# Performance work log

Hardware: AMD Instinct MI355X
Metric: run time of the kernel (lower is better)

## Reference

```python
import jax, jax.numpy as jnp
import numpy as np

N_NODES, N_EDGES, BATCH = 50000, 100000, 256
H = 64            # dim_hidden_features
D_NODE, D_EDGE, D_RBF = 110, 8, 8
D_SET = 2 * H     # Set2Set input_dim = 128, output_dim = 256
D_HID = 512
D_CAT = 54
MP_STEPS, S2S_ITERS = 4, 3


def setup_inputs() -> dict:
    key = jax.random.key(0)
    ks = iter(jax.random.split(key, 48))

    def nrm(shape, s=0.05):
        return jax.random.normal(next(ks), shape, dtype=jnp.float32) * s

    inp = {}
    inp["node_attribute"] = jax.random.normal(next(ks), (N_NODES, D_NODE), dtype=jnp.float32)
    inp["edge_attribute"] = jax.random.normal(next(ks), (N_EDGES, D_EDGE), dtype=jnp.float32)
    inp["edge_length"] = jax.random.uniform(next(ks), (N_EDGES,), dtype=jnp.float32)
    inp["src"] = jax.random.randint(next(ks), (N_EDGES,), 0, N_NODES, dtype=jnp.int32)
    inp["dst"] = jax.random.randint(next(ks), (N_EDGES,), 0, N_NODES, dtype=jnp.int32)
    inp["node_graph"] = jnp.sort(jax.random.randint(next(ks), (N_NODES,), 0, BATCH, dtype=jnp.int32))
    # atom_feature_projector
    inp["proj_W"] = nrm((D_NODE, H)); inp["proj_b"] = jnp.zeros((H,), jnp.float32)
    # RBF layer: centers ~ U(0,1), beta = 10 (per reset_parameters)
    inp["centers"] = jax.random.uniform(next(ks), (D_RBF,), dtype=jnp.float32)
    inp["beta"] = jnp.full((D_RBF,), 10.0, jnp.float32)
    # NNConv edge function: Linear(16 -> 64*64), plus NNConv bias
    inp["bond_W"] = nrm((D_EDGE + D_RBF, H * H)); inp["bond_b"] = jnp.zeros((H * H,), jnp.float32)
    inp["conv_b"] = jnp.zeros((H,), jnp.float32)
    # GRU (input H, hidden H); PyTorch layout (3H, in)
    inp["gru_Wih"] = nrm((3 * H, H)); inp["gru_Whh"] = nrm((3 * H, H))
    inp["gru_bih"] = jnp.zeros((3 * H,), jnp.float32); inp["gru_bhh"] = jnp.zeros((3 * H,), jnp.float32)
    # Set2Set LSTM: input 2*D_SET=256, hidden D_SET=128, 2 layers; PyTorch layout (4H, in)
    inp["lstm_Wih0"] = nrm((4 * D_SET, 2 * D_SET)); inp["lstm_Whh0"] = nrm((4 * D_SET, D_SET))
    inp["lstm_bih0"] = jnp.zeros((4 * D_SET,), jnp.float32); inp["lstm_bhh0"] = jnp.zeros((4 * D_SET,), jnp.float32)
    inp["lstm_Wih1"] = nrm((4 * D_SET, D_SET)); inp["lstm_Whh1"] = nrm((4 * D_SET, D_SET))
    inp["lstm_bih1"] = jnp.zeros((4 * D_SET,), jnp.float32); inp["lstm_bhh1"] = jnp.zeros((4 * D_SET,), jnp.float32)
    # sparsify: Linear(256 -> 512) + PReLU(init 0.25)
    inp["sp_W"] = nrm((2 * D_SET, D_HID)); inp["sp_b"] = jnp.zeros((D_HID,), jnp.float32)
    inp["prelu_a"] = jnp.array([0.25], jnp.float32)
    # catalyst1 head: hiddens[0] (512->512 ReLU, 512->512 Tanh) then outputs[0] (512->54)
    inp["h0_W1"] = nrm((D_HID, D_HID)); inp["h0_b1"] = jnp.zeros((D_HID,), jnp.float32)
    inp["h0_W2"] = nrm((D_HID, D_HID)); inp["h0_b2"] = jnp.zeros((D_HID,), jnp.float32)
    inp["out_W"] = nrm((D_HID, D_CAT)); inp["out_b"] = jnp.zeros((D_CAT,), jnp.float32)
    return inp


def _lstm_cell(x, h, c, Wih, Whh, bih, bhh):
    # PyTorch LSTM gate order: i, f, g, o
    g = x @ Wih.T + bih + h @ Whh.T + bhh
    i, f, gg, o = jnp.split(g, 4, axis=-1)
    c = jax.nn.sigmoid(f) * c + jax.nn.sigmoid(i) * jnp.tanh(gg)
    h = jax.nn.sigmoid(o) * jnp.tanh(c)
    return h, c


def reference(node_attribute, edge_attribute, edge_length, src, dst, node_graph,
              proj_W, proj_b, centers, beta, bond_W, bond_b, conv_b,
              gru_Wih, gru_Whh, gru_bih, gru_bhh,
              lstm_Wih0, lstm_Whh0, lstm_bih0, lstm_bhh0,
              lstm_Wih1, lstm_Whh1, lstm_bih1, lstm_bhh1,
              sp_W, sp_b, prelu_a, h0_W1, h0_b1, h0_W2, h0_b2, out_W, out_b):
    n_nodes = node_attribute.shape[0]
    # atom feature projection
    x = jax.nn.relu(node_attribute @ proj_W + proj_b)                       # (N, H)
    # edge features = [edge_attribute, RBF(length)]
    rbf = jnp.exp(-beta * (edge_length[:, None] - centers[None, :]) ** 2)   # (E, 8)
    efeat = jnp.concatenate([edge_attribute, rbf], axis=-1)                 # (E, 16)
    # NNConv per-edge weight matrix; edge features are constant over MP steps
    W_e = (efeat @ bond_W + bond_b).reshape(-1, H, H)                       # (E, H, H)

    feat, h = x, x
    for _ in range(MP_STEPS):
        # NNConv: message = h_src @ W_e, sum-aggregated at dst, plus bias
        m = jnp.einsum('ei,eio->eo', feat[src], W_e)                        # (E, H)
        agg = jax.ops.segment_sum(m, dst, num_segments=n_nodes) + conv_b    # (N, H)
        gx = jax.nn.relu(agg)
        # GRU cell (PyTorch gate order r, z, n)
        gi = gx @ gru_Wih.T + gru_bih
        gh = h @ gru_Whh.T + gru_bhh
        i_r, i_z, i_n = jnp.split(gi, 3, axis=-1)
        h_r, h_z, h_n = jnp.split(gh, 3, axis=-1)
        r = jax.nn.sigmoid(i_r + h_r)
        z = jax.nn.sigmoid(i_z + h_z)
        n = jnp.tanh(i_n + r * h_n)
        h = (1.0 - z) * n + z * h
        feat = h
    node_agg = jnp.concatenate([feat, x], axis=-1)                          # (N, 2H)

    # Set2Set pooling over graphs (segment softmax attention, 2-layer LSTM)
    B = BATCH
    h0 = c0 = jnp.zeros((B, D_SET), node_agg.dtype)
    h1 = c1 = jnp.zeros((B, D_SET), node_agg.dtype)
    q_star = jnp.zeros((B, 2 * D_SET), node_agg.dtype)
    for _ in range(S2S_ITERS):
        h0, c0 = _lstm_cell(q_star, h0, c0, lstm_Wih0, lstm_Whh0, lstm_bih0, lstm_bhh0)
        h1, c1 = _lstm_cell(h0, h1, c1, lstm_Wih1, lstm_Whh1, lstm_bih1, lstm_bhh1)
        q = h1                                                              # (B, 128)
        e = jnp.sum(node_agg * q[node_graph], axis=-1)                      # (N,)
        emax = jax.ops.segment_max(e, node_graph, num_segments=B)
        p = jnp.exp(e - emax[node_graph])
        denom = jax.ops.segment_sum(p, node_graph, num_segments=B)
        alpha = p / denom[node_graph]                                       # per-graph softmax
        r_out = jax.ops.segment_sum(node_agg * alpha[:, None], node_graph, num_segments=B)
        q_star = jnp.concatenate([q, r_out], axis=-1)                       # (B, 256)

    # sparsify (Linear + PReLU)
    feats = q_star @ sp_W + sp_b                                            # (B, 512)
    feats = jnp.where(feats >= 0, feats, prelu_a * feats)
    # catalyst1 head
    hid = jnp.tanh(jax.nn.relu(feats @ h0_W1 + h0_b1) @ h0_W2 + h0_b2)
    return jax.nn.softmax(hid @ out_W + out_b, axis=-1)                     # (B, 54)
```

## Files before the change

kernel.cpp:

```cpp
#include <hip/hip_runtime.h>
#include <math.h>

constexpr int N = 50000;
constexpr int E = 100000;
constexpr int B = 256;
constexpr int H = 64;
constexpr int DN = 110;
constexpr int NBLK = (E + 63) / 64;

#define DEV __device__ __forceinline__

typedef __attribute__((ext_vector_type(8))) short short8;
typedef __attribute__((ext_vector_type(4))) float floatx4;

DEV float sigf(float x) { return 1.0f / (1.0f + expf(-x)); }

DEV short f2bf(float f) {
    unsigned u = __float_as_uint(f);
    unsigned r = (u + 0x7fffu + ((u >> 16) & 1u)) >> 16;
    return (short)r;
}
DEV float bf2f(short s) { return __uint_as_float(((unsigned)(unsigned short)s) << 16); }

DEV void cvt8(const float* p, short8& hi, short8& lo) {
    float4 u0 = *(const float4*)p;
    float4 u1 = *(const float4*)(p + 4);
    float vv[8] = {u0.x, u0.y, u0.z, u0.w, u1.x, u1.y, u1.z, u1.w};
#pragma unroll
    for (int j = 0; j < 8; ++j) {
        short hb = f2bf(vv[j]);
        hi[j] = hb;
        lo[j] = f2bf(vv[j] - bf2f(hb));
    }
}

__global__ void k_izero(int* p, int n) {
    int i = blockIdx.x * 256 + threadIdx.x;
    if (i < n) p[i] = 0;
}

DEV void d_packpair(const float* __restrict__ in, float* __restrict__ out, int IN_I, int idx) {
    int i = idx >> 8;
    int j = idx & 255;
    out[2 * idx]     = in[(size_t)j * IN_I + i];
    out[2 * idx + 1] = in[(size_t)(j + 256) * IN_I + i];
}

DEV void d_prepB(const float* __restrict__ W, short* __restrict__ out,
                 int NT16, int ld, int trans, int ocap, int kcap, int idx) {
    int lane = idx & 63;
    int t = idx >> 6;
    int ntile = t % NT16;
    int kt = t / NT16;
    int quad = lane >> 4, col = lane & 15;
    int o = ntile * 16 + col;
    short hi[8], lo[8];
#pragma unroll
    for (int j = 0; j < 8; ++j) {
        int k = kt * 32 + quad * 8 + j;
        float v = 0.0f;
        if (o < ocap && k < kcap) v = trans ? W[(size_t)o * ld + k] : W[(size_t)k * ld + o];
        short hb = f2bf(v);
        hi[j] = hb;
        lo[j] = f2bf(v - bf2f(hb));
    }
    short* dh = out + (((size_t)(t * 2 + 0) * 64 + lane) * 8);
    short* dl = out + (((size_t)(t * 2 + 1) * 64 + lane) * 8);
#pragma unroll
    for (int j = 0; j < 8; ++j) { dh[j] = hi[j]; dl[j] = lo[j]; }
}

DEV void d_prepW(const float* __restrict__ bond_W, const float* __restrict__ bond_b,
                 short* __restrict__ wf, int idx) {
    int lane = idx & 63;
    int t = idx >> 6;
    int ks = t & 1;
    int nt = (t >> 1) & 3;
    int kk = t >> 3;
    const float* S = (kk < 16) ? (bond_W + kk * 4096) : bond_b;
    int quad = lane >> 4, col = lane & 15;
    short hi[8], lo[8];
#pragma unroll
    for (int j = 0; j < 8; ++j) {
        int i = ks * 32 + quad * 8 + j;
        float v = S[i * 64 + nt * 16 + col];
        short hb = f2bf(v);
        hi[j] = hb;
        lo[j] = f2bf(v - bf2f(hb));
    }
    short* dh = wf + (((size_t)(t * 2 + 0) * 64 + lane) * 8);
    short* dl = wf + (((size_t)(t * 2 + 1) * 64 + lane) * 8);
#pragma unroll
    for (int j = 0; j < 8; ++j) { dh[j] = hi[j]; dl[j] = lo[j]; }
}

__launch_bounds__(256)
__global__ void k_prep0(const float* lWih0, const float* lWhh0, const float* lWih1, const float* lWhh1,
                        float* lW0P, float* lU0P, float* lW1P, float* lU1P,
                        const float* bond_W, const float* bond_b, short* wf,
                        const float* gru_Wih, const float* gru_Whh, short* fgI, short* fgH,
                        const float* proj_W, short* fproj,
                        const float* ea, const float* el, const float* centers,
                        const float* beta, const int* epos, float* ef_t,
                        const int* ng, int* gs, int* ge,
                        float* zreg) {
    int idx = blockIdx.x * 256 + threadIdx.x;
    if (idx < 65536) { d_packpair(lWih0, lW0P, 256, idx); return; }
    idx -= 65536;
    if (idx < 32768) { d_packpair(lWhh0, lU0P, 128, idx); return; }
    idx -= 32768;
    if (idx < 32768) { d_packpair(lWih1, lW1P, 128, idx); return; }
    idx -= 32768;
    if (idx < 32768) { d_packpair(lWhh1, lU1P, 128, idx); return; }
    idx -= 32768;
    if (idx < 8704) { d_prepW(bond_W, bond_b, wf, idx); return; }
    idx -= 8704;
    if (idx < 1536) { d_prepB(gru_Wih, fgI, 12, 64, 1, 192, 64, idx); return; }
    idx -= 1536;
    if (idx < 1536) { d_prepB(gru_Whh, fgH, 12, 64, 1, 192, 64, idx); return; }
    idx -= 1536;
    if (idx < 1024) { d_prepB(proj_W, fproj, 4, 64, 0, 64, DN, idx); return; }
    idx -= 1024;
    if (idx < E) {
        int e = idx;
        int pos = epos[e];
        float L = el[e];
#pragma unroll
        for (int j = 0; j < 8; ++j) ef_t[(size_t)j * E + pos] = ea[e * 8 + j];
#pragma unroll
        for (int j = 0; j < 8; ++j) {
            float d = L - centers[j];
            ef_t[(size_t)(8 + j) * E + pos] = expf(-beta[j] * d * d);
        }
        ef_t[(size_t)16 * E + pos] = 1.0f;
        return;
    }
    idx -= E;
    if (idx < N) {
        int n = idx;
        int g = ng[n];
        int gp = (n == 0) ? -1 : ng[n - 1];
        if (g != gp) {
            gs[g] = n;
            if (n > 0) ge[gp] = n;
            for (int q = gp + 1; q < g; ++q) { gs[q] = 0; ge[q] = 0; }
        }
        if (n == N - 1) {
            ge[g] = N;
            for (int q = g + 1; q < B; ++q) { gs[q] = 0; ge[q] = 0; }
        }
        return;
    }
    idx -= N;
    if (idx < 196608) { zreg[idx] = 0.0f; return; }
}
constexpr int PREP0_TOTAL = 65536 + 3 * 32768 + 8704 + 2 * 1536 + 1024 + E + N + 196608;

__launch_bounds__(256)
__global__ void k_prephead(const float* sp_W, short* fsp, const float* h0_W1, short* fw1,
                           const float* h0_W2, short* fw2, const float* out_W, short* fow) {
    int idx = blockIdx.x * 256 + threadIdx.x;
    if (idx < 16384) { d_prepB(sp_W, fsp, 32, 512, 0, 512, 256, idx); return; }
    idx -= 16384;
    if (idx < 32768) { d_prepB(h0_W1, fw1, 32, 512, 0, 512, 512, idx); return; }
    idx -= 32768;
    if (idx < 32768) { d_prepB(h0_W2, fw2, 32, 512, 0, 512, 512, idx); return; }
    idx -= 32768;
    if (idx < 4096) { d_prepB(out_W, fow, 4, 54, 0, 54, 512, idx); return; }
}
constexpr int PREPH_TOTAL = 16384 + 2 * 32768 + 4096;

__global__ void k_deg(const int* __restrict__ dst, int* __restrict__ deg) {
    int e = blockIdx.x * 256 + threadIdx.x;
    if (e < E) atomicAdd(&deg[dst[e]], 1);
}
__global__ void k_scan1(const int* __restrict__ deg, int* __restrict__ bsum) {
    __shared__ int s[256];
    int b = blockIdx.x, tid = threadIdx.x;
    int idx = b * 256 + tid;
    s[tid] = (idx < N) ? deg[idx] : 0;
    __syncthreads();
    for (int st = 128; st > 0; st >>= 1) {
        if (tid < st) s[tid] += s[tid + st];
        __syncthreads();
    }
    if (tid == 0) bsum[b] = s[0];
}
__global__ void k_scan2p(int* __restrict__ bsum, int nb) {
    __shared__ int s[256];
    int tid = threadIdx.x;
    int v = (tid < nb) ? bsum[tid] : 0;
    s[tid] = v;
    __syncthreads();
    for (int off = 1; off < 256; off <<= 1) {
        int t = (tid >= off) ? s[tid - off] : 0;
        __syncthreads();
        s[tid] += t;
        __syncthreads();
    }
    if (tid < nb) bsum[tid] = s[tid] - v;
}
__global__ void k_scan3(const int* __restrict__ deg, const int* __restrict__ bsum,
                        int* __restrict__ cursor, int* __restrict__ roff) {
    __shared__ int s[256];
    int b = blockIdx.x, tid = threadIdx.x;
    int idx = b * 256 + tid;
    int v = (idx < N) ? deg[idx] : 0;
    s[tid] = v;
    __syncthreads();
    for (int off = 1; off < 256; off <<= 1) {
        int t = (tid >= off) ? s[tid - off] : 0;
        __syncthreads();
        s[tid] += t;
        __syncthreads();
    }
    if (idx < N) {
        int start = bsum[b] + s[tid] - v;
        cursor[idx] = start;
        roff[idx] = start;
    }
    if (idx == 0) roff[N] = E;
}
__global__ void k_scat(const int* __restrict__ src, const int* __restrict__ dst,
                       int* __restrict__ cursor, int* __restrict__ srcp,
                       int* __restrict__ epos, int* __restrict__ dstp) {
    int e = blockIdx.x * 256 + threadIdx.x;
    if (e >= E) return;
    int d = dst[e];
    int pos = atomicAdd(&cursor[d], 1);
    srcp[pos] = src[e];
    dstp[pos] = d;
    epos[e] = pos;
}

__launch_bounds__(256)
__global__ void k_projm(const float* __restrict__ na, const short* __restrict__ fp,
                        const float* __restrict__ b, float* __restrict__ x,
                        short* __restrict__ hs) {
    __shared__ float as[16 * 132];
    int tid = threadIdx.x, lane = tid & 63, nt = tid >> 6;
    int quad = lane >> 4, col = lane & 15;
    int s0 = blockIdx.x * 16;
    for (int i = tid; i < 16 * DN; i += 256) {
        int r = i / DN, c = i % DN;
        as[r * 132 + c] = na[(size_t)s0 * DN + i];
    }
    for (int i = tid; i < 16 * 22; i += 256) {
        int r = i / 22, c = DN + i % 22;
        as[r * 132 + c] = 0.0f;
    }
    __syncthreads();
    const short8* F = (const short8*)fp;
    floatx4 T = {0.0f, 0.0f, 0.0f, 0.0f};
#pragma unroll
    for (int kt = 0; kt < 4; ++kt) {
        const float* ap = as + col * 132 + kt * 32 + quad * 8;
        short8 ah, al;
#pragma unroll
        for (int j = 0; j < 8; ++j) {
            float v = ap[j];
            short hb = f2bf(v);
            ah[j] = hb;
            al[j] = f2bf(v - bf2f(hb));
        }
        int t = kt * 4 + nt;
        short8 bh = F[(t * 2 + 0) * 64 + lane];
        short8 bl = F[(t * 2 + 1) * 64 + lane];
        T = __builtin_amdgcn_mfma_f32_16x16x32_bf16(ah, bh, T, 0, 0, 0);
        T = __builtin_amdgcn_mfma_f32_16x16x32_bf16(al, bh, T, 0, 0, 0);
        T = __builtin_amdgcn_mfma_f32_16x16x32_bf16(ah, bl, T, 0, 0, 0);
    }
    int o = nt * 16 + col;
    float bo = b[o];
#pragma unroll
    for (int r = 0; r < 4; ++r) {
        int n = s0 + quad * 4 + r;
        float v = fmaxf(T[r] + bo, 0.0f);
        x[(size_t)n * 64 + o] = v;
        short hb = f2bf(v);
        hs[(size_t)n * 128 + o] = hb;
        hs[(size_t)n * 128 + 64 + o] = f2bf(v - bf2f(hb));
    }
}

__launch_bounds__(256)
__global__ void k_msgagg(const short* __restrict__ hs, const float* __restrict__ ef_t,
                         const short* __restrict__ wf, const int* __restrict__ srcp,
                         const int* __restrict__ dstp,
                         float* __restrict__ agg, float* __restrict__ bpart) {
    __shared__ int dsh[64];
    __shared__ int shprev;
    __shared__ float Csh[64][68];

    int tid = threadIdx.x;
    int e0 = blockIdx.x * 64;
    int lane = tid & 63;
    int nt = tid >> 6;
    int quad = lane >> 4, col = lane & 15;

    if (tid < 64) {
        int eg = e0 + tid;
        dsh[tid] = (eg < E) ? dstp[eg] : N;
    }
    if (tid == 0) shprev = (e0 == 0) ? -1 : dstp[e0 - 1];

    short8 Ah[4][2], Al[4][2];
#pragma unroll
    for (int mt = 0; mt < 4; ++mt) {
        int eg = e0 + mt * 16 + col;
        int s = (eg < E) ? srcp[eg] : 0;
        const short* hp = hs + (size_t)s * 128 + quad * 8;
#pragma unroll
        for (int ks = 0; ks < 2; ++ks) {
            Ah[mt][ks] = *(const short8*)(hp + ks * 32);
            Al[mt][ks] = *(const short8*)(hp + 64 + ks * 32);
        }
    }

    const short8* Wf = (const short8*)wf;
    const float* efb = ef_t + e0 + quad * 4;
    float C[4][4] = {};

#define LOADB(d0, d1, d2, d3, KK)                      \
    {                                                  \
        int tb_ = ((KK) * 4 + nt) * 2;                 \
        d0 = Wf[((tb_ + 0) * 2 + 0) * 64 + lane];      \
        d1 = Wf[((tb_ + 1) * 2 + 0) * 64 + lane];      \
        d2 = Wf[((tb_ + 0) * 2 + 1) * 64 + lane];      \
        d3 = Wf[((tb_ + 1) * 2 + 1) * 64 + lane];      \
    }

    short8 c0, c1, c2, c3, n0_, n1_, n2_, n3_, q0, q1, q2, q3;
    LOADB(c0, c1, c2, c3, 0);
    LOADB(n0_, n1_, n2_, n3_, 1);
    LOADB(q0, q1, q2, q3, 2);

#pragma unroll 1
    for (int kk = 0; kk < 17; ++kk) {
        int kn = kk + 3;
        if (kn > 16) kn = 16;
        short8 p0, p1, p2, p3;
        LOADB(p0, p1, p2, p3, kn);

        float4 ef0 = *(const float4*)(efb + (size_t)kk * E + 0);
        float4 ef1 = *(const float4*)(efb + (size_t)kk * E + 16);
        float4 ef2 = *(const float4*)(efb + (size_t)kk * E + 32);
        float4 ef3 = *(const float4*)(efb + (size_t)kk * E + 48);
        float4 efv[4] = {ef0, ef1, ef2, ef3};

#pragma unroll
        for (int mt = 0; mt < 4; ++mt) {
            floatx4 T = {0.0f, 0.0f, 0.0f, 0.0f};
            T = __builtin_amdgcn_mfma_f32_16x16x32_bf16(Ah[mt][0], c0, T, 0, 0, 0);
            T = __builtin_amdgcn_mfma_f32_16x16x32_bf16(Ah[mt][1], c1, T, 0, 0, 0);
            T = __builtin_amdgcn_mfma_f32_16x16x32_bf16(Al[mt][0], c0, T, 0, 0, 0);
            T = __builtin_amdgcn_mfma_f32_16x16x32_bf16(Al[mt][1], c1, T, 0, 0, 0);
            T = __builtin_amdgcn_mfma_f32_16x16x32_bf16(Ah[mt][0], c2, T, 0, 0, 0);
            T = __builtin_amdgcn_mfma_f32_16x16x32_bf16(Ah[mt][1], c3, T, 0, 0, 0);
            C[mt][0] += efv[mt].x * T[0];
            C[mt][1] += efv[mt].y * T[1];
            C[mt][2] += efv[mt].z * T[2];
            C[mt][3] += efv[mt].w * T[3];
        }
        c0 = n0_; c1 = n1_; c2 = n2_; c3 = n3_;
        n0_ = q0; n1_ = q1; n2_ = q2; n3_ = q3;
        q0 = p0; q1 = p1; q2 = p2; q3 = p3;
    }
#undef LOADB

#pragma unroll
    for (int mt = 0; mt < 4; ++mt)
#pragma unroll
        for (int r = 0; r < 4; ++r)
            Csh[mt * 16 + quad * 4 + r][nt * 16 + col] = C[mt][r];
    __syncthreads();

    if (tid < 64) {
        int c = tid;
        int prevd = shprev;
        int firstd = dsh[0];
        for (int q = prevd + 1; q < firstd; ++q) agg[(size_t)q * 64 + c] = 0.0f;
        int cur = firstd;
        float acc = 0.0f;
        bool owned = (e0 == 0) || (firstd != prevd);
        bool done = false;
        for (int r = 0; r < 64; ++r) {
            int d = dsh[r];
            if (d != cur) {
                if (owned) agg[(size_t)cur * 64 + c] = acc;
                else bpart[(size_t)blockIdx.x * 64 + c] = acc;
                int dc = (d < N) ? d : N;
                for (int q = cur + 1; q < dc; ++q) agg[(size_t)q * 64 + c] = 0.0f;
                cur = d;
                acc = 0.0f;
                owned = true;
                if (cur >= N) { done = true; break; }
            }
            acc += Csh[r][c];
        }
        if (!done) {
            if (owned) agg[(size_t)cur * 64 + c] = acc;
            else bpart[(size_t)blockIdx.x * 64 + c] = acc;
        }
    }
}

__launch_bounds__(256)
__global__ void k_gru4(const float* agg, const float* __restrict__ bpart,
                       const int* __restrict__ roff, const float* __restrict__ conv_b,
                       short* __restrict__ hs,
                       const short* __restrict__ fI, const short* __restrict__ fH,
                       const float* __restrict__ bih, const float* __restrict__ bhh,
                       float* hf) {
    __shared__ float aggS[32 * 65];
    __shared__ short hsS[32 * 132];
    int tid = threadIdx.x, lane = tid & 63, nt = tid >> 6;
    int quad = lane >> 4, col = lane & 15;
    int n0 = blockIdx.x * 32;

    {
        const float* src = agg + (size_t)n0 * 64;
#pragma unroll
        for (int it = 0; it < 2; ++it) {
            int i = tid * 4 + it * 1024;
            float4 v = {0.0f, 0.0f, 0.0f, 0.0f};
            if ((size_t)n0 * 64 + i + 3 < (size_t)N * 64) v = *(const float4*)(src + i);
            int r = i >> 6, c = i & 63;
            *(float4*)&aggS[r * 65 + c] = v;
        }
        const short* hsrc = hs + (size_t)n0 * 128;
#pragma unroll
        for (int it = 0; it < 2; ++it) {
            int i = tid * 8 + it * 2048;
            short8 v = short8{0, 0, 0, 0, 0, 0, 0, 0};
            if ((size_t)n0 * 128 + i + 7 < (size_t)N * 128) v = *(const short8*)(hsrc + i);
            int r = i >> 7, c = i & 127;
            *(short8*)&hsS[r * 132 + c] = v;
        }
    }
    __syncthreads();

    short8 Gh[2][2], Gl[2][2], Hh[2][2], Hl[2][2];
#pragma unroll
    for (int mt = 0; mt < 2; ++mt) {
        int node = n0 + mt * 16 + col;
        bool ok = node < N;
        int row = mt * 16 + col;
        float acc[2][8];
        const float* ag = &aggS[row * 65];
#pragma unroll
        for (int ks = 0; ks < 2; ++ks) {
            const float* cb = conv_b + ks * 32 + quad * 8;
            float4 a0 = *(const float4*)(ag + ks * 32 + quad * 8);
            float4 a1 = *(const float4*)(ag + ks * 32 + quad * 8 + 4);
            acc[ks][0] = a0.x + cb[0]; acc[ks][1] = a0.y + cb[1];
            acc[ks][2] = a0.z + cb[2]; acc[ks][3] = a0.w + cb[3];
            acc[ks][4] = a1.x + cb[4]; acc[ks][5] = a1.y + cb[5];
            acc[ks][6] = a1.z + cb[6]; acc[ks][7] = a1.w + cb[7];
        }
        int rs = ok ? roff[node] : 0;
        int re = ok ? roff[node + 1] : 0;
        if (re > rs) {
            int b0 = rs >> 6, b1 = (re - 1) >> 6;
            for (int bb = b0 + 1; bb <= b1; ++bb) {
                const float* bp = bpart + (size_t)bb * 64;
#pragma unroll
                for (int ks = 0; ks < 2; ++ks) {
                    float4 p0 = *(const float4*)(bp + ks * 32 + quad * 8);
                    float4 p1 = *(const float4*)(bp + ks * 32 + quad * 8 + 4);
                    acc[ks][0] += p0.x; acc[ks][1] += p0.y;
                    acc[ks][2] += p0.z; acc[ks][3] += p0.w;
                    acc[ks][4] += p1.x; acc[ks][5] += p1.y;
                    acc[ks][6] += p1.z; acc[ks][7] += p1.w;
                }
            }
        }
        const short* hp = &hsS[row * 132];
#pragma unroll
        for (int ks = 0; ks < 2; ++ks) {
            Hh[mt][ks] = *(const short8*)(hp + ks * 32);
            Hl[mt][ks] = *(const short8*)(hp + 64 + ks * 32);
#pragma unroll
            for (int j = 0; j < 8; ++j) {
                float g = ok ? fmaxf(acc[ks][j], 0.0f) : 0.0f;
                short gb = f2bf(g);
                Gh[mt][ks][j] = gb;
                Gl[mt][ks][j] = f2bf(g - bf2f(gb));
            }
        }
    }
    __syncthreads();

    const short8* FI = (const short8*)fI;
    const short8* FH = (const short8*)fH;
    floatx4 aI[2][3] = {}, aH[2][3] = {};
#pragma unroll
    for (int ks = 0; ks < 2; ++ks) {
        short8 bIh[3], bIl[3], bHh[3], bHl[3];
#pragma unroll
        for (int g = 0; g < 3; ++g) {
            int t = ks * 12 + g * 4 + nt;
            bIh[g] = FI[(t * 2 + 0) * 64 + lane];
            bIl[g] = FI[(t * 2 + 1) * 64 + lane];
            bHh[g] = FH[(t * 2 + 0) * 64 + lane];
            bHl[g] = FH[(t * 2 + 1) * 64 + lane];
        }
#pragma unroll
        for (int mt = 0; mt < 2; ++mt) {
#pragma unroll
            for (int g = 0; g < 3; ++g) {
                aI[mt][g] = __builtin_amdgcn_mfma_f32_16x16x32_bf16(Gh[mt][ks], bIh[g], aI[mt][g], 0, 0, 0);
                aI[mt][g] = __builtin_amdgcn_mfma_f32_16x16x32_bf16(Gl[mt][ks], bIh[g], aI[mt][g], 0, 0, 0);
                aI[mt][g] = __builtin_amdgcn_mfma_f32_16x16x32_bf16(Gh[mt][ks], bIl[g], aI[mt][g], 0, 0, 0);
                aH[mt][g] = __builtin_amdgcn_mfma_f32_16x16x32_bf16(Hh[mt][ks], bHh[g], aH[mt][g], 0, 0, 0);
                aH[mt][g] = __builtin_amdgcn_mfma_f32_16x16x32_bf16(Hl[mt][ks], bHh[g], aH[mt][g], 0, 0, 0);
                aH[mt][g] = __builtin_amdgcn_mfma_f32_16x16x32_bf16(Hh[mt][ks], bHl[g], aH[mt][g], 0, 0, 0);
            }
        }
    }

    int o = nt * 16 + col;
    float br = bih[o], bz = bih[64 + o], bn = bih[128 + o];
    float cr = bhh[o], cz = bhh[64 + o], cn = bhh[128 + o];
#pragma unroll
    for (int mt = 0; mt < 2; ++mt) {
#pragma unroll
        for (int r = 0; r < 4; ++r) {
            int row = mt * 16 + quad * 4 + r;
            float rg = sigf(aI[mt][0][r] + br + aH[mt][0][r] + cr);
            float z  = sigf(aI[mt][1][r] + bz + aH[mt][1][r] + cz);
            float ng = tanhf(aI[mt][2][r] + bn + rg * (aH[mt][2][r] + cn));
            float hold = bf2f(hsS[row * 132 + o]) + bf2f(hsS[row * 132 + 64 + o]);
            aggS[row * 65 + o] = (1.0f - z) * ng + z * hold;
        }
    }
    __syncthreads();

#pragma unroll
    for (int it = 0; it < 2; ++it) {
        int i = tid * 8 + it * 2048;
        int r = i >> 7, c = i & 127;
        int node = n0 + r;
        if (node < N) {
            bool hiP = (c < 64);
            int f0 = hiP ? c : (c - 64);
            short8 v;
#pragma unroll
            for (int j = 0; j < 8; ++j) {
                float hv = aggS[r * 65 + f0 + j];
                short hb = f2bf(hv);
                v[j] = hiP ? hb : f2bf(hv - bf2f(hb));
            }
            *(short8*)(hs + (size_t)node * 128 + c) = v;
        }
    }
    if (hf) {
#pragma unroll
        for (int it = 0; it < 2; ++it) {
            int i = tid * 4 + it * 1024;
            int r = i >> 6, c = i & 63;
            int node = n0 + r;
            if (node < N)
                *(float4*)(hf + (size_t)node * 64 + c) = *(const float4*)&aggS[r * 65 + c];
        }
    }
}

__launch_bounds__(256)
__global__ void k_s2s(float* __restrict__ h0, float* __restrict__ c0,
                      float* __restrict__ h1, float* __restrict__ c1,
                      float* __restrict__ q_star,
                      const float* __restrict__ W0P, const float* __restrict__ U0P,
                      const float* __restrict__ b0i, const float* __restrict__ b0h,
                      const float* __restrict__ W1P, const float* __restrict__ U1P,
                      const float* __restrict__ b1i, const float* __restrict__ b1h,
                      const float* __restrict__ hf, const float* __restrict__ x,
                      const int* __restrict__ gs, const int* __restrict__ ge) {
    __shared__ float xb[256], hb[128], gb[512], h0n[128], qv[128];
    __shared__ float mrg[4][2][64];
    __shared__ float ml[4][2];
    int g = blockIdx.x, tid = threadIdx.x;
    xb[tid] = q_star[g * 256 + tid];
    if (tid < 128) hb[tid] = h0[g * 128 + tid];
    __syncthreads();
    float g0 = b0i[tid] + b0h[tid];
    float g1 = b0i[tid + 256] + b0h[tid + 256];
    for (int i = 0; i < 256; ++i) {
        float xx = xb[i];
        float2 w = *(const float2*)(W0P + 2 * (i * 256 + tid));
        g0 += xx * w.x;
        g1 += xx * w.y;
    }
    for (int i = 0; i < 128; ++i) {
        float hh = hb[i];
        float2 w = *(const float2*)(U0P + 2 * (i * 256 + tid));
        g0 += hh * w.x;
        g1 += hh * w.y;
    }
    gb[tid] = g0; gb[tid + 256] = g1;
    __syncthreads();
    if (tid < 128) {
        float ii = gb[tid], ff = gb[128 + tid], gg = gb[256 + tid], oo = gb[384 + tid];
        float c = sigf(ff) * c0[g * 128 + tid] + sigf(ii) * tanhf(gg);
        float hn = sigf(oo) * tanhf(c);
        c0[g * 128 + tid] = c; h0[g * 128 + tid] = hn; h0n[tid] = hn;
        hb[tid] = h1[g * 128 + tid];
    }
    __syncthreads();
    float ga = b1i[tid] + b1h[tid];
    float gbv = b1i[tid + 256] + b1h[tid + 256];
    for (int i = 0; i < 128; ++i) {
        float xx = h0n[i], hh = hb[i];
        float2 w1 = *(const float2*)(W1P + 2 * (i * 256 + tid));
        float2 u1 = *(const float2*)(U1P + 2 * (i * 256 + tid));
        ga  += xx * w1.x + hh * u1.x;
        gbv += xx * w1.y + hh * u1.y;
    }
    gb[tid] = ga; gb[tid + 256] = gbv;
    __syncthreads();
    if (tid < 128) {
        float ii = gb[tid], ff = gb[128 + tid], gg = gb[256 + tid], oo = gb[384 + tid];
        float c = sigf(ff) * c1[g * 128 + tid] + sigf(ii) * tanhf(gg);
        float hn = sigf(oo) * tanhf(c);
        c1[g * 128 + tid] = c; h1[g * 128 + tid] = hn;
        q_star[g * 256 + tid] = hn;
        qv[tid] = hn;
    }
    __syncthreads();
    int s0v = gs[g], s1v = ge[g];
    int lane = tid & 63, grp = tid >> 6;
    float qh = qv[lane], qx = qv[64 + lane];
    float mM = -INFINITY, lL = 0.0f, nh = 0.0f, nx = 0.0f;
    for (int n = s0v + grp; n < s1v; n += 16) {
        float hv[4], xv[4], e[4];
#pragma unroll
        for (int j = 0; j < 4; ++j) {
            int nj = n + 4 * j;
            int nc = (nj < s1v) ? nj : n;
            hv[j] = hf[(size_t)nc * 64 + lane];
            xv[j] = x[(size_t)nc * 64 + lane];
            e[j] = hv[j] * qh + xv[j] * qx;
        }
#pragma unroll
        for (int off = 32; off; off >>= 1) {
#pragma unroll
            for (int j = 0; j < 4; ++j) e[j] += __shfl_xor(e[j], off, 64);
        }
#pragma unroll
        for (int j = 0; j < 4; ++j)
            if (n + 4 * j >= s1v) e[j] = -INFINITY;
        float mb = fmaxf(fmaxf(e[0], e[1]), fmaxf(e[2], e[3]));
        float mn = fmaxf(mM, mb);
        float sc = expf(mM - mn);
        float w0 = expf(e[0] - mn), w1 = expf(e[1] - mn);
        float w2 = expf(e[2] - mn), w3 = expf(e[3] - mn);
        lL = lL * sc + ((w0 + w1) + (w2 + w3));
        nh = nh * sc + ((w0 * hv[0] + w1 * hv[1]) + (w2 * hv[2] + w3 * hv[3]));
        nx = nx * sc + ((w0 * xv[0] + w1 * xv[1]) + (w2 * xv[2] + w3 * xv[3]));
        mM = mn;
    }
    mrg[grp][0][lane] = nh;
    mrg[grp][1][lane] = nx;
    if (lane == 0) { ml[grp][0] = mM; ml[grp][1] = lL; }
    __syncthreads();
    if (tid < 128) {
        int half = tid >> 6, dl = tid & 63;
        float M = -INFINITY;
#pragma unroll
        for (int i = 0; i < 4; ++i) M = fmaxf(M, ml[i][0]);
        float L = 0.0f, NUM = 0.0f;
#pragma unroll
        for (int i = 0; i < 4; ++i) {
            float sc = expf(ml[i][0] - M);
            L += ml[i][1] * sc;
            NUM += mrg[i][half][dl] * sc;
        }
        q_star[g * 256 + 128 + tid] = (s1v > s0v) ? NUM / L : 0.0f;
    }
}

template<int MODE>
__launch_bounds__(256)
__global__ void k_hgemm(const float* __restrict__ A, const short* __restrict__ Bf,
                        const float* __restrict__ bias, const float* __restrict__ pa,
                        float* __restrict__ Cout, int K, int NT16) {
    int tid = threadIdx.x, lane = tid & 63, nt = tid >> 6;
    int quad = lane >> 4, col = lane & 15;
    int s0 = blockIdx.x * 16;
    int ntile = blockIdx.y * 4 + nt;
    int NoutTot = NT16 * 16;
    const short8* F = (const short8*)Bf;
    floatx4 T = {0.0f, 0.0f, 0.0f, 0.0f};
    const float* ap = A + (size_t)(s0 + col) * K + quad * 8;
    int KT = K >> 5;
#pragma unroll 4
    for (int kt = 0; kt < KT; ++kt) {
        short8 ah, al;
        cvt8(ap + kt * 32, ah, al);
        int t = kt * NT16 + ntile;
        short8 bh = F[(t * 2 + 0) * 64 + lane];
        short8 bl = F[(t * 2 + 1) * 64 + lane];
        T = __builtin_amdgcn_mfma_f32_16x16x32_bf16(ah, bh, T, 0, 0, 0);
        T = __builtin_amdgcn_mfma_f32_16x16x32_bf16(al, bh, T, 0, 0, 0);
        T = __builtin_amdgcn_mfma_f32_16x16x32_bf16(ah, bl, T, 0, 0, 0);
    }
    int o = ntile * 16 + col;
    float b = bias[o];
    float a = (MODE == 0) ? pa[0] : 0.0f;
#pragma unroll
    for (int r = 0; r < 4; ++r) {
        float v = T[r] + b;
        if (MODE == 0) v = (v >= 0.0f) ? v : a * v;
        if (MODE == 1) v = fmaxf(v, 0.0f);
        if (MODE == 2) v = tanhf(v);
        Cout[(size_t)(s0 + quad * 4 + r) * NoutTot + o] = v;
    }
}

__launch_bounds__(256)
__global__ void k_hout(const float* __restrict__ A, const short* __restrict__ Bf,
                       const float* __restrict__ ob, float* __restrict__ out) {
    __shared__ float sm[16][64];
    __shared__ float smax[16], sinv[16];
    int tid = threadIdx.x, lane = tid & 63, nt = tid >> 6;
    int quad = lane >> 4, col = lane & 15;
    int s0 = blockIdx.x * 16;
    const short8* F = (const short8*)Bf;
    floatx4 T = {0.0f, 0.0f, 0.0f, 0.0f};
    const float* ap = A + (size_t)(s0 + col) * 512 + quad * 8;
#pragma unroll 4
    for (int kt = 0; kt < 16; ++kt) {
        short8 ah, al;
        cvt8(ap + kt * 32, ah, al);
        int t = kt * 4 + nt;
        short8 bh = F[(t * 2 + 0) * 64 + lane];
        short8 bl = F[(t * 2 + 1) * 64 + lane];
        T = __builtin_amdgcn_mfma_f32_16x16x32_bf16(ah, bh, T, 0, 0, 0);
        T = __builtin_amdgcn_mfma_f32_16x16x32_bf16(al, bh, T, 0, 0, 0);
        T = __builtin_amdgcn_mfma_f32_16x16x32_bf16(ah, bl, T, 0, 0, 0);
    }
    int o = nt * 16 + col;
    float b = (o < 54) ? ob[o] : 0.0f;
#pragma unroll
    for (int r = 0; r < 4; ++r)
        sm[quad * 4 + r][o] = (o < 54) ? (T[r] + b) : -1e30f;
    __syncthreads();
    if (tid < 16) {
        float m = -INFINITY;
        for (int j = 0; j < 54; ++j) m = fmaxf(m, sm[tid][j]);
        float s = 0.0f;
        for (int j = 0; j < 54; ++j) s += expf(sm[tid][j] - m);
        smax[tid] = m;
        sinv[tid] = 1.0f / s;
    }
    __syncthreads();
    for (int idx = tid; idx < 16 * 54; idx += 256) {
        int srow = idx / 54, oo = idx % 54;
        out[(size_t)(s0 + srow) * 54 + oo] = expf(sm[srow][oo] - smax[srow]) * sinv[srow];
    }
}

extern "C" void kernel_launch(void* const* d_in, const int* in_sizes, int n_in,
                              void* d_out, int out_size, void* d_ws, size_t ws_size,
                              hipStream_t stream) {
    const float* node_attr = (const float*)d_in[0];
    const float* edge_attr = (const float*)d_in[1];
    const float* edge_len  = (const float*)d_in[2];
    const int*   src       = (const int*)d_in[3];
    const int*   dst       = (const int*)d_in[4];
    const int*   node_grph = (const int*)d_in[5];
    const float* proj_W    = (const float*)d_in[6];
    const float* proj_b    = (const float*)d_in[7];
    const float* centers   = (const float*)d_in[8];
    const float* beta      = (const float*)d_in[9];
    const float* bond_W    = (const float*)d_in[10];
    const float* bond_b    = (const float*)d_in[11];
    const float* conv_b    = (const float*)d_in[12];
    const float* gru_Wih   = (const float*)d_in[13];
    const float* gru_Whh   = (const float*)d_in[14];
    const float* gru_bih   = (const float*)d_in[15];
    const float* gru_bhh   = (const float*)d_in[16];
    const float* lWih0     = (const float*)d_in[17];
    const float* lWhh0     = (const float*)d_in[18];
    const float* lbih0     = (const float*)d_in[19];
    const float* lbhh0     = (const float*)d_in[20];
    const float* lWih1     = (const float*)d_in[21];
    const float* lWhh1     = (const float*)d_in[22];
    const float* lbih1     = (const float*)d_in[23];
    const float* lbhh1     = (const float*)d_in[24];
    const float* sp_W      = (const float*)d_in[25];
    const float* sp_b      = (const float*)d_in[26];
    const float* prelu_a   = (const float*)d_in[27];
    const float* h0_W1     = (const float*)d_in[28];
    const float* h0_b1     = (const float*)d_in[29];
    const float* h0_W2     = (const float*)d_in[30];
    const float* h0_b2     = (const float*)d_in[31];
    const float* out_W     = (const float*)d_in[32];
    const float* out_b     = (const float*)d_in[33];
    float* out = (float*)d_out;

    float* ws = (float*)d_ws;
    size_t off = 0;
    float* x      = ws + off; off += (size_t)N * 64;
    float* hsf    = ws + off; off += (size_t)N * 64;
    float* ef_t   = ws + off; off += (size_t)E * 17;
    float* agg    = ws + off; off += (size_t)N * 64;
    float* wfrag  = ws + off; off += 17 * 16 * 64 * 8 / 2;
    float* fgI    = ws + off; off += 2 * 64 * 192 / 2;
    float* fgH    = ws + off; off += 2 * 64 * 192 / 2;
    float* fproj  = ws + off; off += 16 * 1024 / 2;
    float* lW0P   = ws + off; off += 256 * 512;
    float* lU0P   = ws + off; off += 128 * 512;
    float* lW1P   = ws + off; off += 128 * 512;
    float* lU1P   = ws + off; off += 128 * 512;
    float* h0     = ws + off; off += B * 128;
    float* c0     = ws + off; off += B * 128;
    float* h1     = ws + off; off += B * 128;
    float* c1     = ws + off; off += B * 128;
    float* q_star = ws + off; off += B * 256;
    float* bpart  = ws + off; off += (size_t)NBLK * 64;
    int* gs       = (int*)(ws + off); off += B;
    int* ge       = (int*)(ws + off); off += B;
    int* deg      = (int*)(ws + off); off += N;
    int* cursor   = (int*)(ws + off); off += N;
    int* roff     = (int*)(ws + off); off += N + 1;
    int* bsum     = (int*)(ws + off); off += 256;
    int* srcp     = (int*)(ws + off); off += E;
    int* epos     = (int*)(ws + off); off += E;
    int* dstp     = (int*)(ws + off); off += E;

    short* hs = (short*)hsf;

    short* fsp = (short*)ef_t;
    short* fw1 = (short*)(ef_t + 131072);
    short* fw2 = (short*)(ef_t + 131072 + 262144);
    short* fow = (short*)(ef_t + 131072 + 2 * 262144);
    float* hb1 = ef_t + 131072 + 2 * 262144 + 32768;
    float* hb2 = hb1 + 131072;

    constexpr int NB = (N + 255) / 256;

    k_izero<<<NB, 256, 0, stream>>>(deg, N);
    k_deg<<<(E + 255) / 256, 256, 0, stream>>>(dst, deg);
    k_scan1<<<NB, 256, 0, stream>>>(deg, bsum);
    k_scan2p<<<1, 256, 0, stream>>>(bsum, NB);
    k_scan3<<<NB, 256, 0, stream>>>(deg, bsum, cursor, roff);
    k_scat<<<(E + 255) / 256, 256, 0, stream>>>(src, dst, cursor, srcp, epos, dstp);

    k_prep0<<<(PREP0_TOTAL + 255) / 256, 256, 0, stream>>>(
        lWih0, lWhh0, lWih1, lWhh1, lW0P, lU0P, lW1P, lU1P,
        bond_W, bond_b, (short*)wfrag, gru_Wih, gru_Whh, (short*)fgI, (short*)fgH,
        proj_W, (short*)fproj,
        edge_attr, edge_len, centers, beta, epos, ef_t,
        node_grph, gs, ge, h0);

    k_projm<<<N / 16, 256, 0, stream>>>(node_attr, (const short*)fproj, proj_b, x, hs);

    for (int step = 0; step < 4; ++step) {
        k_msgagg<<<NBLK, 256, 0, stream>>>(hs, ef_t, (const short*)wfrag, srcp, dstp,
                                           agg, bpart);
        k_gru4<<<(N + 31) / 32, 256, 0, stream>>>(agg, bpart, roff, conv_b, hs,
                                                  (const short*)fgI, (const short*)fgH,
                                                  gru_bih, gru_bhh,
                                                  (step == 3) ? agg : nullptr);
    }

    k_prephead<<<(PREPH_TOTAL + 255) / 256, 256, 0, stream>>>(
        sp_W, fsp, h0_W1, fw1, h0_W2, fw2, out_W, fow);

    for (int it = 0; it < 3; ++it) {
        k_s2s<<<B, 256, 0, stream>>>(h0, c0, h1, c1, q_star,
                                     lW0P, lU0P, lbih0, lbhh0,
                                     lW1P, lU1P, lbih1, lbhh1,
                                     agg, x, gs, ge);
    }

    k_hgemm<0><<<dim3(16, 8), 256, 0, stream>>>(q_star, fsp, sp_b, prelu_a, hb1, 256, 32);
    k_hgemm<1><<<dim3(16, 8), 256, 0, stream>>>(hb1, fw1, h0_b1, nullptr, hb2, 512, 32);
    k_hgemm<2><<<dim3(16, 8), 256, 0, stream>>>(hb2, fw2, h0_b2, nullptr, hb1, 512, 32);
    k_hout<<<16, 256, 0, stream>>>(hb1, fow, out_b, out);
}
```

Baseline: 696.6 us.

## Fuse Set2Set iterations and head weight prep into one kernel; stage edge features in LDS

The three Set2Set launches become a single kernel that keeps the LSTM state in shared memory, skips the matmuls against the zero initial state on the first iteration, and drops the separate zeroing of the state buffers. The head weight packing moves into the tail of that kernel, removing the k_prephead launch. In message aggregation, the per-block edge features and source indices are first loaded into LDS with coalesced loads before the MFMA loop. The trade-off is an extra block-wide barrier and more shared memory in k_msgagg, which may lower occupancy.

```diff
diff --git a/kernel.cpp b/kernel.cpp
--- a/kernel.cpp
+++ b/kernel.cpp
@@ -102,8 +102,7 @@
                         const float* proj_W, short* fproj,
                         const float* ea, const float* el, const float* centers,
                         const float* beta, const int* epos, float* ef_t,
-                        const int* ng, int* gs, int* ge,
-                        float* zreg) {
+                        const int* ng, int* gs, int* ge) {
     int idx = blockIdx.x * 256 + threadIdx.x;
     if (idx < 65536) { d_packpair(lWih0, lW0P, 256, idx); return; }
     idx -= 65536;
@@ -151,24 +150,8 @@
         }
         return;
     }
-    idx -= N;
-    if (idx < 196608) { zreg[idx] = 0.0f; return; }
-}
-constexpr int PREP0_TOTAL = 65536 + 3 * 32768 + 8704 + 2 * 1536 + 1024 + E + N + 196608;
-
-__launch_bounds__(256)
-__global__ void k_prephead(const float* sp_W, short* fsp, const float* h0_W1, short* fw1,
-                           const float* h0_W2, short* fw2, const float* out_W, short* fow) {
-    int idx = blockIdx.x * 256 + threadIdx.x;
-    if (idx < 16384) { d_prepB(sp_W, fsp, 32, 512, 0, 512, 256, idx); return; }
-    idx -= 16384;
-    if (idx < 32768) { d_prepB(h0_W1, fw1, 32, 512, 0, 512, 512, idx); return; }
-    idx -= 32768;
-    if (idx < 32768) { d_prepB(h0_W2, fw2, 32, 512, 0, 512, 512, idx); return; }
-    idx -= 32768;
-    if (idx < 4096) { d_prepB(out_W, fow, 4, 54, 0, 54, 512, idx); return; }
-}
-constexpr int PREPH_TOTAL = 16384 + 2 * 32768 + 4096;
+}
+constexpr int PREP0_TOTAL = 65536 + 3 * 32768 + 8704 + 2 * 1536 + 1024 + E + N;
 
 __global__ void k_deg(const int* __restrict__ dst, int* __restrict__ deg) {
     int e = blockIdx.x * 256 + threadIdx.x;
@@ -288,6 +271,8 @@
                          const short* __restrict__ wf, const int* __restrict__ srcp,
                          const int* __restrict__ dstp,
                          float* __restrict__ agg, float* __restrict__ bpart) {
+    __shared__ float efs[17 * 64];
+    __shared__ int srcs[64];
     __shared__ int dsh[64];
     __shared__ int shprev;
     __shared__ float Csh[64][68];
@@ -300,15 +285,21 @@
 
     if (tid < 64) {
         int eg = e0 + tid;
+        srcs[tid] = (eg < E) ? srcp[eg] : 0;
         dsh[tid] = (eg < E) ? dstp[eg] : N;
     }
     if (tid == 0) shprev = (e0 == 0) ? -1 : dstp[e0 - 1];
+    for (int i = tid; i < 17 * 64; i += 256) {
+        int kk = i >> 6, e = i & 63;
+        int eg = e0 + e;
+        efs[i] = (eg < E) ? ef_t[(size_t)kk * E + eg] : 0.0f;
+    }
+    __syncthreads();
 
     short8 Ah[4][2], Al[4][2];
 #pragma unroll
     for (int mt = 0; mt < 4; ++mt) {
-        int eg = e0 + mt * 16 + col;
-        int s = (eg < E) ? srcp[eg] : 0;
+        int s = srcs[mt * 16 + col];
         const short* hp = hs + (size_t)s * 128 + quad * 8;
 #pragma unroll
         for (int ks = 0; ks < 2; ++ks) {
@@ -318,7 +309,6 @@
     }
 
     const short8* Wf = (const short8*)wf;
-    const float* efb = ef_t + e0 + quad * 4;
     float C[4][4] = {};
 
 #define LOADB(d0, d1, d2, d3, KK)                      \
@@ -341,12 +331,6 @@
         if (kn > 16) kn = 16;
         short8 p0, p1, p2, p3;
         LOADB(p0, p1, p2, p3, kn);
-
-        float4 ef0 = *(const float4*)(efb + (size_t)kk * E + 0);
-        float4 ef1 = *(const float4*)(efb + (size_t)kk * E + 16);
-        float4 ef2 = *(const float4*)(efb + (size_t)kk * E + 32);
-        float4 ef3 = *(const float4*)(efb + (size_t)kk * E + 48);
-        float4 efv[4] = {ef0, ef1, ef2, ef3};
 
 #pragma unroll
         for (int mt = 0; mt < 4; ++mt) {
@@ -357,10 +341,11 @@
             T = __builtin_amdgcn_mfma_f32_16x16x32_bf16(Al[mt][1], c1, T, 0, 0, 0);
             T = __builtin_amdgcn_mfma_f32_16x16x32_bf16(Ah[mt][0], c2, T, 0, 0, 0);
             T = __builtin_amdgcn_mfma_f32_16x16x32_bf16(Ah[mt][1], c3, T, 0, 0, 0);
-            C[mt][0] += efv[mt].x * T[0];
-            C[mt][1] += efv[mt].y * T[1];
-            C[mt][2] += efv[mt].z * T[2];
-            C[mt][3] += efv[mt].w * T[3];
+            float4 ef = *(const float4*)&efs[kk * 64 + mt * 16 + quad * 4];
+            C[mt][0] += ef.x * T[0];
+            C[mt][1] += ef.y * T[1];
+            C[mt][2] += ef.z * T[2];
+            C[mt][3] += ef.w * T[3];
         }
         c0 = n0_; c1 = n1_; c2 = n2_; c3 = n3_;
         n0_ = q0; n1_ = q1; n2_ = q2; n3_ = q3;
@@ -567,115 +552,139 @@
 }
 
 __launch_bounds__(256)
-__global__ void k_s2s(float* __restrict__ h0, float* __restrict__ c0,
-                      float* __restrict__ h1, float* __restrict__ c1,
-                      float* __restrict__ q_star,
-                      const float* __restrict__ W0P, const float* __restrict__ U0P,
-                      const float* __restrict__ b0i, const float* __restrict__ b0h,
-                      const float* __restrict__ W1P, const float* __restrict__ U1P,
-                      const float* __restrict__ b1i, const float* __restrict__ b1h,
-                      const float* __restrict__ hf, const float* __restrict__ x,
-                      const int* __restrict__ gs, const int* __restrict__ ge) {
-    __shared__ float xb[256], hb[128], gb[512], h0n[128], qv[128];
+__global__ void k_s2s3(float* __restrict__ q_star,
+                       const float* __restrict__ W0P, const float* __restrict__ U0P,
+                       const float* __restrict__ b0i, const float* __restrict__ b0h,
+                       const float* __restrict__ W1P, const float* __restrict__ U1P,
+                       const float* __restrict__ b1i, const float* __restrict__ b1h,
+                       const float* __restrict__ hf, const float* __restrict__ x,
+                       const int* __restrict__ gs, const int* __restrict__ ge,
+                       const float* sp_W, short* fsp, const float* h0_W1, short* fw1,
+                       const float* h0_W2, short* fw2, const float* out_W, short* fow) {
+    __shared__ float xb[256], h0b[128], c0b[128], h1b[128], c1b[128];
+    __shared__ float gb[512], h0n[128], qv[128];
     __shared__ float mrg[4][2][64];
     __shared__ float ml[4][2];
     int g = blockIdx.x, tid = threadIdx.x;
-    xb[tid] = q_star[g * 256 + tid];
-    if (tid < 128) hb[tid] = h0[g * 128 + tid];
-    __syncthreads();
-    float g0 = b0i[tid] + b0h[tid];
-    float g1 = b0i[tid + 256] + b0h[tid + 256];
-    for (int i = 0; i < 256; ++i) {
-        float xx = xb[i];
-        float2 w = *(const float2*)(W0P + 2 * (i * 256 + tid));
-        g0 += xx * w.x;
-        g1 += xx * w.y;
-    }
-    for (int i = 0; i < 128; ++i) {
-        float hh = hb[i];
-        float2 w = *(const float2*)(U0P + 2 * (i * 256 + tid));
-        g0 += hh * w.x;
-        g1 += hh * w.y;
-    }
-    gb[tid] = g0; gb[tid + 256] = g1;
-    __syncthreads();
-    if (tid < 128) {
-        float ii = gb[tid], ff = gb[128 + tid], gg = gb[256 + tid], oo = gb[384 + tid];
-        float c = sigf(ff) * c0[g * 128 + tid] + sigf(ii) * tanhf(gg);
-        float hn = sigf(oo) * tanhf(c);
-        c0[g * 128 + tid] = c; h0[g * 128 + tid] = hn; h0n[tid] = hn;
-        hb[tid] = h1[g * 128 + tid];
-    }
-    __syncthreads();
-    float ga = b1i[tid] + b1h[tid];
-    float gbv = b1i[tid + 256] + b1h[tid + 256];
-    for (int i = 0; i < 128; ++i) {
-        float xx = h0n[i], hh = hb[i];
-        float2 w1 = *(const float2*)(W1P + 2 * (i * 256 + tid));
-        float2 u1 = *(const float2*)(U1P + 2 * (i * 256 + tid));
-        ga  += xx * w1.x + hh * u1.x;
-        gbv += xx * w1.y + hh * u1.y;
-    }
-    gb[tid] = ga; gb[tid + 256] = gbv;
-    __syncthreads();
-    if (tid < 128) {
-        float ii = gb[tid], ff = gb[128 + tid], gg = gb[256 + tid], oo = gb[384 + tid];
-        float c = sigf(ff) * c1[g * 128 + tid] + sigf(ii) * tanhf(gg);
-        float hn = sigf(oo) * tanhf(c);
-        c1[g * 128 + tid] = c; h1[g * 128 + tid] = hn;
-        q_star[g * 256 + tid] = hn;
-        qv[tid] = hn;
-    }
-    __syncthreads();
+    int lane = tid & 63, grp = tid >> 6;
     int s0v = gs[g], s1v = ge[g];
-    int lane = tid & 63, grp = tid >> 6;
-    float qh = qv[lane], qx = qv[64 + lane];
-    float mM = -INFINITY, lL = 0.0f, nh = 0.0f, nx = 0.0f;
-    for (int n = s0v + grp; n < s1v; n += 16) {
-        float hv[4], xv[4], e[4];
-#pragma unroll
-        for (int j = 0; j < 4; ++j) {
-            int nj = n + 4 * j;
-            int nc = (nj < s1v) ? nj : n;
-            hv[j] = hf[(size_t)nc * 64 + lane];
-            xv[j] = x[(size_t)nc * 64 + lane];
-            e[j] = hv[j] * qh + xv[j] * qx;
-        }
-#pragma unroll
-        for (int off = 32; off; off >>= 1) {
-#pragma unroll
-            for (int j = 0; j < 4; ++j) e[j] += __shfl_xor(e[j], off, 64);
-        }
-#pragma unroll
-        for (int j = 0; j < 4; ++j)
-            if (n + 4 * j >= s1v) e[j] = -INFINITY;
-        float mb = fmaxf(fmaxf(e[0], e[1]), fmaxf(e[2], e[3]));
-        float mn = fmaxf(mM, mb);
-        float sc = expf(mM - mn);
-        float w0 = expf(e[0] - mn), w1 = expf(e[1] - mn);
-        float w2 = expf(e[2] - mn), w3 = expf(e[3] - mn);
-        lL = lL * sc + ((w0 + w1) + (w2 + w3));
-        nh = nh * sc + ((w0 * hv[0] + w1 * hv[1]) + (w2 * hv[2] + w3 * hv[3]));
-        nx = nx * sc + ((w0 * xv[0] + w1 * xv[1]) + (w2 * xv[2] + w3 * xv[3]));
-        mM = mn;
-    }
-    mrg[grp][0][lane] = nh;
-    mrg[grp][1][lane] = nx;
-    if (lane == 0) { ml[grp][0] = mM; ml[grp][1] = lL; }
-    __syncthreads();
-    if (tid < 128) {
-        int half = tid >> 6, dl = tid & 63;
-        float M = -INFINITY;
-#pragma unroll
-        for (int i = 0; i < 4; ++i) M = fmaxf(M, ml[i][0]);
-        float L = 0.0f, NUM = 0.0f;
-#pragma unroll
-        for (int i = 0; i < 4; ++i) {
-            float sc = expf(ml[i][0] - M);
-            L += ml[i][1] * sc;
-            NUM += mrg[i][half][dl] * sc;
-        }
-        q_star[g * 256 + 128 + tid] = (s1v > s0v) ? NUM / L : 0.0f;
+    xb[tid] = 0.0f;
+    if (tid < 128) { h0b[tid] = 0.0f; c0b[tid] = 0.0f; h1b[tid] = 0.0f; c1b[tid] = 0.0f; }
+    __syncthreads();
+
+    for (int it = 0; it < 3; ++it) {
+        float g0 = b0i[tid] + b0h[tid];
+        float g1 = b0i[tid + 256] + b0h[tid + 256];
+        if (it > 0) {
+            for (int i = 0; i < 256; ++i) {
+                float xx = xb[i];
+                float2 w = *(const float2*)(W0P + 2 * (i * 256 + tid));
+                g0 += xx * w.x;
+                g1 += xx * w.y;
+            }
+            for (int i = 0; i < 128; ++i) {
+                float hh = h0b[i];
+                float2 w = *(const float2*)(U0P + 2 * (i * 256 + tid));
+                g0 += hh * w.x;
+                g1 += hh * w.y;
+            }
+        }
+        gb[tid] = g0; gb[tid + 256] = g1;
+        __syncthreads();
+        if (tid < 128) {
+            float ii = gb[tid], ff = gb[128 + tid], gg = gb[256 + tid], oo = gb[384 + tid];
+            float c = sigf(ff) * c0b[tid] + sigf(ii) * tanhf(gg);
+            float hn = sigf(oo) * tanhf(c);
+            c0b[tid] = c; h0b[tid] = hn; h0n[tid] = hn;
+        }
+        __syncthreads();
+        float ga = b1i[tid] + b1h[tid];
+        float gbv = b1i[tid + 256] + b1h[tid + 256];
+        for (int i = 0; i < 128; ++i) {
+            float xx = h0n[i];
+            float2 w1 = *(const float2*)(W1P + 2 * (i * 256 + tid));
+            ga += xx * w1.x;
+            gbv += xx * w1.y;
+        }
+        if (it > 0) {
+            for (int i = 0; i < 128; ++i) {
+                float hh = h1b[i];
+                float2 u1 = *(const float2*)(U1P + 2 * (i * 256 + tid));
+                ga += hh * u1.x;
+                gbv += hh * u1.y;
+            }
+        }
+        gb[tid] = ga; gb[tid + 256] = gbv;
+        __syncthreads();
+        if (tid < 128) {
+            float ii = gb[tid], ff = gb[128 + tid], gg = gb[256 + tid], oo = gb[384 + tid];
+            float c = sigf(ff) * c1b[tid] + sigf(ii) * tanhf(gg);
+            float hn = sigf(oo) * tanhf(c);
+            c1b[tid] = c; h1b[tid] = hn; qv[tid] = hn;
+        }
+        __syncthreads();
+        float qh = qv[lane], qx = qv[64 + lane];
+        float mM = -INFINITY, lL = 0.0f, nh = 0.0f, nx = 0.0f;
+        for (int n = s0v + grp; n < s1v; n += 16) {
+            float hv[4], xv[4], e[4];
+#pragma unroll
+            for (int j = 0; j < 4; ++j) {
+                int nj = n + 4 * j;
+                int nc = (nj < s1v) ? nj : n;
+                hv[j] = hf[(size_t)nc * 64 + lane];
+                xv[j] = x[(size_t)nc * 64 + lane];
+                e[j] = hv[j] * qh + xv[j] * qx;
+            }
+#pragma unroll
+            for (int off = 32; off; off >>= 1) {
+#pragma unroll
+                for (int j = 0; j < 4; ++j) e[j] += __shfl_xor(e[j], off, 64);
+            }
+#pragma unroll
+            for (int j = 0; j < 4; ++j)
+                if (n + 4 * j >= s1v) e[j] = -INFINITY;
+            float mb = fmaxf(fmaxf(e[0], e[1]), fmaxf(e[2], e[3]));
+            float mn = fmaxf(mM, mb);
+            float sc = expf(mM - mn);
+            float w0 = expf(e[0] - mn), w1 = expf(e[1] - mn);
+            float w2 = expf(e[2] - mn), w3 = expf(e[3] - mn);
+            lL = lL * sc + ((w0 + w1) + (w2 + w3));
+            nh = nh * sc + ((w0 * hv[0] + w1 * hv[1]) + (w2 * hv[2] + w3 * hv[3]));
+            nx = nx * sc + ((w0 * xv[0] + w1 * xv[1]) + (w2 * xv[2] + w3 * xv[3]));
+            mM = mn;
+        }
+        mrg[grp][0][lane] = nh;
+        mrg[grp][1][lane] = nx;
+        if (lane == 0) { ml[grp][0] = mM; ml[grp][1] = lL; }
+        __syncthreads();
+        if (tid < 128) {
+            int half = tid >> 6, dl = tid & 63;
+            float M = -INFINITY;
+#pragma unroll
+            for (int i = 0; i < 4; ++i) M = fmaxf(M, ml[i][0]);
+            float L = 0.0f, NUM = 0.0f;
+#pragma unroll
+            for (int i = 0; i < 4; ++i) {
+                float sc = expf(ml[i][0] - M);
+                L += ml[i][1] * sc;
+                NUM += mrg[i][half][dl] * sc;
+            }
+            xb[128 + tid] = (s1v > s0v) ? NUM / L : 0.0f;
+            xb[tid] = qv[tid];
+        }
+        __syncthreads();
+    }
+    q_star[g * 256 + tid] = xb[tid];
+
+    for (int ii2 = tid; ii2 < 336; ii2 += 256) {
+        int idx = g * 336 + ii2;
+        if (idx < 16384) { d_prepB(sp_W, fsp, 32, 512, 0, 512, 256, idx); continue; }
+        idx -= 16384;
+        if (idx < 32768) { d_prepB(h0_W1, fw1, 32, 512, 0, 512, 512, idx); continue; }
+        idx -= 32768;
+        if (idx < 32768) { d_prepB(h0_W2, fw2, 32, 512, 0, 512, 512, idx); continue; }
+        idx -= 32768;
+        d_prepB(out_W, fow, 4, 54, 0, 54, 512, idx);
     }
 }
 
@@ -813,10 +822,6 @@
     float* lU0P   = ws + off; off += 128 * 512;
     float* lW1P   = ws + off; off += 128 * 512;
     float* lU1P   = ws + off; off += 128 * 512;
-    float* h0     = ws + off; off += B * 128;
-    float* c0     = ws + off; off += B * 128;
-    float* h1     = ws + off; off += B * 128;
-    float* c1     = ws + off; off += B * 128;
     float* q_star = ws + off; off += B * 256;
     float* bpart  = ws + off; off += (size_t)NBLK * 64;
     int* gs       = (int*)(ws + off); off += B;
@@ -852,7 +857,7 @@
         bond_W, bond_b, (short*)wfrag, gru_Wih, gru_Whh, (short*)fgI, (short*)fgH,
         proj_W, (short*)fproj,
         edge_attr, edge_len, centers, beta, epos, ef_t,
-        node_grph, gs, ge, h0);
+        node_grph, gs, ge);
 
     k_projm<<<N / 16, 256, 0, stream>>>(node_attr, (const short*)fproj, proj_b, x, hs);
 
@@ -865,15 +870,11 @@
                                                   (step == 3) ? agg : nullptr);
     }
 
-    k_prephead<<<(PREPH_TOTAL + 255) / 256, 256, 0, stream>>>(
-        sp_W, fsp, h0_W1, fw1, h0_W2, fw2, out_W, fow);
-
-    for (int it = 0; it < 3; ++it) {
-        k_s2s<<<B, 256, 0, stream>>>(h0, c0, h1, c1, q_star,
-                                     lW0P, lU0P, lbih0, lbhh0,
-                                     lW1P, lU1P, lbih1, lbhh1,
-                                     agg, x, gs, ge);
-    }
+    k_s2s3<<<B, 256, 0, stream>>>(q_star,
+                                  lW0P, lU0P, lbih0, lbhh0,
+                                  lW1P, lU1P, lbih1, lbhh1,
+                                  agg, x, gs, ge,
+                                  sp_W, fsp, h0_W1, fw1, h0_W2, fw2, out_W, fow);
 
     k_hgemm<0><<<dim3(16, 8), 256, 0, stream>>>(q_star, fsp, sp_b, prelu_a, hb1, 256, 32);
     k_hgemm<1><<<dim3(16, 8), 256, 0, stream>>>(hb1, fw1, h0_b1, nullptr, hb2, 512, 32);
```

New measurement: 671.2 us. 3.6% less time.
